# Kernel tuning notes

Hardware: AMD Instinct MI355X
Metric: run time of the kernel (lower is better)

Reference implementation:

```python
import jax, jax.numpy as jnp
import numpy as np

N_DRUG = 20000
N_DIS = 20000
D = 128
E = 640000
L = 200000


def _sage(x_src, x_dst, src, dst, Wl, Wr, b, n_dst):
    # SAGEConv: out_i = lin_l(mean_{j in N(i)} x_src_j) + lin_r(x_dst_i)
    msg = x_src[src]                                   # [E, D] gather
    agg = jax.ops.segment_sum(msg, dst, num_segments=n_dst)
    cnt = jax.ops.segment_sum(jnp.ones((src.shape[0],), x_src.dtype), dst,
                              num_segments=n_dst)
    mean = agg / jnp.maximum(cnt, 1.0)[:, None]
    return mean @ Wl + b + x_dst @ Wr


def setup_inputs() -> dict:
    key = jax.random.key(0)
    ks = jax.random.split(key, 24)
    s = 1.0 / np.sqrt(D)
    inp = {
        "x_drug": jax.random.normal(ks[0], (N_DRUG, D), jnp.float32),
        "x_disease": jax.random.normal(ks[1], (N_DIS, D), jnp.float32),
        "ei_d2s": jax.random.randint(ks[2], (2, E), 0, 20000),
        "ei_s2d": jax.random.randint(ks[3], (2, E), 0, 20000),
        "edge_label_index": jax.random.randint(ks[4], (2, L), 0, 20000),
    }
    names = ["W1l_d2s", "W1r_d2s", "W1l_s2d", "W1r_s2d",
             "W2l_d2s", "W2r_d2s", "W2l_s2d", "W2r_s2d"]
    for i, n in enumerate(names):
        inp[n] = jax.random.uniform(ks[5 + i], (D, D), jnp.float32, -s, s)
    for i, n in enumerate(["b1_d2s", "b1_s2d", "b2_d2s", "b2_s2d"]):
        inp[n] = jax.random.uniform(ks[13 + i], (D,), jnp.float32, -s, s)
    inp["dec_W1"] = jax.random.uniform(ks[17], (2 * D, D), jnp.float32, -s, s)
    inp["dec_b1"] = jax.random.uniform(ks[18], (D,), jnp.float32, -s, s)
    inp["dec_W2"] = jax.random.uniform(ks[19], (D, 1), jnp.float32, -s, s)
    inp["dec_b2"] = jax.random.uniform(ks[20], (1,), jnp.float32, -s, s)
    return inp


def reference(x_drug, x_disease,
              W1l_d2s, W1r_d2s, b1_d2s, W1l_s2d, W1r_s2d, b1_s2d,
              W2l_d2s, W2r_d2s, b2_d2s, W2l_s2d, W2r_s2d, b2_s2d,
              dec_W1, dec_b1, dec_W2, dec_b2,
              ei_d2s, ei_s2d, edge_label_index):
    # --- hetero GNN encoder, layer 1 (relu) ---
    h_dis = jax.nn.relu(_sage(x_drug, x_disease, ei_d2s[0], ei_d2s[1],
                              W1l_d2s, W1r_d2s, b1_d2s, N_DIS))
    h_drug = jax.nn.relu(_sage(x_disease, x_drug, ei_s2d[0], ei_s2d[1],
                               W1l_s2d, W1r_s2d, b1_s2d, N_DRUG))
    # --- layer 2 (no activation) ---
    z_dis = _sage(h_drug, h_dis, ei_d2s[0], ei_d2s[1],
                  W2l_d2s, W2r_d2s, b2_d2s, N_DIS)
    z_drug = _sage(h_dis, h_drug, ei_s2d[0], ei_s2d[1],
                   W2l_s2d, W2r_s2d, b2_s2d, N_DRUG)
    # --- edge decoder: gather, concat, 2-layer MLP ---
    row, col = edge_label_index[0], edge_label_index[1]
    z = jnp.concatenate([z_drug[row], z_dis[col]], axis=-1)   # [L, 2D]
    z = jax.nn.relu(z @ dec_W1 + dec_b1)
    z = z @ dec_W2 + dec_b2
    return z.reshape(-1)
```

## Files before the change

kernel.cpp:

```cpp
#include <hip/hip_runtime.h>
#include <hip/hip_fp16.h>

#define D 128
#define NDRUG 20000
#define NDIS 20000
#define EDGES 640000
#define LROWS 200000

typedef unsigned short u16;


__device__ inline void h8_load(uint4 u, float f[8]) {
    float2 a = __half22float2(*(const __half2*)&u.x);
    float2 b = __half22float2(*(const __half2*)&u.y);
    float2 c = __half22float2(*(const __half2*)&u.z);
    float2 d = __half22float2(*(const __half2*)&u.w);
    f[0] = a.x; f[1] = a.y; f[2] = b.x; f[3] = b.y;
    f[4] = c.x; f[5] = c.y; f[6] = d.x; f[7] = d.y;
}

__global__ __launch_bounds__(256) void rank2_kernel(
    const int* __restrict__ dA, int* __restrict__ cA, int* __restrict__ rA,
    const int* __restrict__ dB, int* __restrict__ cB, int* __restrict__ rB, int n)
{
    int i = blockIdx.x * blockDim.x + threadIdx.x;
    if (i < n) rA[i] = atomicAdd(&cA[dA[i]], 1);
    else if (i - n < n) rB[i - n] = atomicAdd(&cB[dB[i - n]], 1);
}

__global__ __launch_bounds__(1024) void scan2_kernel(int* __restrict__ c0, int* __restrict__ o0,
                                                     int* __restrict__ c1, int* __restrict__ o1,
                                                     int n) {
    int* cnt_io = (blockIdx.x == 0) ? c0 : c1;
    int* off    = (blockIdx.x == 0) ? o0 : o1;
    __shared__ int wsum[16];
    __shared__ int carry_s;
    const int tid = threadIdx.x;
    const int lane = tid & 63;
    const int wid = tid >> 6;
    if (tid == 0) { carry_s = 0; off[0] = 0; }
    __syncthreads();
    for (int start = 0; start < n; start += 1024) {
        int i = start + tid;
        int v = (i < n) ? cnt_io[i] : 0;
        int carry = carry_s;
        int s = v;
        #pragma unroll
        for (int o = 1; o < 64; o <<= 1) {
            int t = __shfl_up(s, o, 64);
            if (lane >= o) s += t;
        }
        if (lane == 63) wsum[wid] = s;
        __syncthreads();
        if (wid == 0) {
            int ws = (lane < 16) ? wsum[lane] : 0;
            #pragma unroll
            for (int o = 1; o < 16; o <<= 1) {
                int t = __shfl_up(ws, o, 64);
                if (lane >= o) ws += t;
            }
            if (lane < 16) wsum[lane] = ws;
        }
        __syncthreads();
        int woff = (wid > 0) ? wsum[wid - 1] : 0;
        int incl = s + woff + carry;
        if (i < n) {
            off[i + 1] = incl;
            cnt_io[i] = incl - v;
        }
        __syncthreads();
        if (tid == 1023) carry_s = incl;
        __syncthreads();
    }
}

#define SB 104

__global__ __launch_bounds__(256) void scatter_sliced_kernel(
    const int* __restrict__ srcA, const int* __restrict__ dstA,
    const int* __restrict__ rkA, const int* __restrict__ offA, u16* __restrict__ csrA,
    const int* __restrict__ srcB, const int* __restrict__ dstB,
    const int* __restrict__ rkB, const int* __restrict__ offB, u16* __restrict__ csrB,
    int n)
{
    int b = blockIdx.x;
    int dirB = (b >= 8 * SB);
    int bb = b - (dirB ? 8 * SB : 0);
    int s = bb & 7;
    int sub = bb >> 3;
    const int* src = dirB ? srcB : srcA;
    const int* dst = dirB ? dstB : dstA;
    const int* rk  = dirB ? rkB : rkA;
    const int* off = dirB ? offB : offA;
    u16* csr = dirB ? csrB : csrA;

    const int lo = s * 2500, hi = lo + 2500;
    const int chunk = (n + SB - 1) / SB;
    int i0 = sub * chunk;
    int i1 = i0 + chunk; i1 = i1 < n ? i1 : n;
    for (int i = i0 + threadIdx.x; i < i1; i += 256) {
        int d = dst[i];
        if (d >= lo && d < hi) {
            int pos = off[d] + rk[i];
            csr[pos] = (u16)src[i];
        }
    }
}


__global__ __launch_bounds__(256) void cvt16_kernel(const float* __restrict__ in,
                                                    __half* __restrict__ out, int n4) {
    int i = blockIdx.x * blockDim.x + threadIdx.x;
    if (i >= n4) return;
    float4 v = ((const float4*)in)[i];
    __half2 a = __floats2half2_rn(v.x, v.y);
    __half2 b = __floats2half2_rn(v.z, v.w);
    uint2 u;
    u.x = *(unsigned*)&a;
    u.y = *(unsigned*)&b;
    ((uint2*)out)[i] = u;
}

__global__ __launch_bounds__(256) void cvtw_kernel(
    const float* __restrict__ s0, const float* __restrict__ s1,
    const float* __restrict__ s2, const float* __restrict__ s3,
    const float* __restrict__ s4, const float* __restrict__ s5,
    const float* __restrict__ s6, const float* __restrict__ s7,
    const float* __restrict__ s8, const float* __restrict__ s9,
    __half* __restrict__ out)
{
    const int chunk = blockIdx.x >> 4;
    const float* src;
    switch (chunk) {
        case 0: src = s0; break; case 1: src = s1; break;
        case 2: src = s2; break; case 3: src = s3; break;
        case 4: src = s4; break; case 5: src = s5; break;
        case 6: src = s6; break; case 7: src = s7; break;
        case 8: src = s8; break; default: src = s9; break;
    }
    const int i4 = (blockIdx.x & 15) * 256 + threadIdx.x;
    float4 v = ((const float4*)src)[i4];
    __half2 a = __floats2half2_rn(v.x, v.y);
    __half2 b = __floats2half2_rn(v.z, v.w);
    uint2 u;
    u.x = *(unsigned*)&a;
    u.y = *(unsigned*)&b;
    ((uint2*)(out + (size_t)chunk * 16384))[i4] = u;
}


#define NPW 4

__device__ inline void sage_gather(
    const __half* __restrict__ xsrc, const __half* __restrict__ xdst,
    const int* __restrict__ off, const u16* __restrict__ csr,
    float lmean[4][NPW][D], float ldst[4][NPW][D],
    int node0, int ndst, int wid, int lane)
{
    const bool hiHalf = lane >= 32;
    const int lq = lane & 31;
    const int c0 = lq * 4;
    for (int r = 0; r < NPW; ++r) {
        int node = node0 + r;
        if (node >= ndst) break;
        int e0 = off[node], e1 = off[node + 1];
        int deg = e1 - e0;
        float a0 = 0.f, a1 = 0.f, a2 = 0.f, a3 = 0.f;
        for (int base = e0; base < e1; base += 64) {
            int nv = e1 - base; nv = nv < 64 ? nv : 64;
            int myidx = 0;
            if (lane < nv) myidx = csr[base + lane];
            int npair = nv >> 1;
            int t = 0;
            for (; t + 4 <= npair; t += 4) {
                int pa0 = __builtin_amdgcn_readlane(myidx, 2 * t + 0);
                int pb0 = __builtin_amdgcn_readlane(myidx, 2 * t + 1);
                int pa1 = __builtin_amdgcn_readlane(myidx, 2 * t + 2);
                int pb1 = __builtin_amdgcn_readlane(myidx, 2 * t + 3);
                int pa2 = __builtin_amdgcn_readlane(myidx, 2 * t + 4);
                int pb2 = __builtin_amdgcn_readlane(myidx, 2 * t + 5);
                int pa3 = __builtin_amdgcn_readlane(myidx, 2 * t + 6);
                int pb3 = __builtin_amdgcn_readlane(myidx, 2 * t + 7);
                int s0 = hiHalf ? pb0 : pa0;
                int s1 = hiHalf ? pb1 : pa1;
                int s2 = hiHalf ? pb2 : pa2;
                int s3 = hiHalf ? pb3 : pa3;
                uint2 u0 = *(const uint2*)(xsrc + (size_t)s0 * D + c0);
                uint2 u1 = *(const uint2*)(xsrc + (size_t)s1 * D + c0);
                uint2 u2 = *(const uint2*)(xsrc + (size_t)s2 * D + c0);
                uint2 u3 = *(const uint2*)(xsrc + (size_t)s3 * D + c0);
                float2 t0, t1;
                t0 = __half22float2(*(const __half2*)&u0.x);
                t1 = __half22float2(*(const __half2*)&u0.y);
                a0 += t0.x; a1 += t0.y; a2 += t1.x; a3 += t1.y;
                t0 = __half22float2(*(const __half2*)&u1.x);
                t1 = __half22float2(*(const __half2*)&u1.y);
                a0 += t0.x; a1 += t0.y; a2 += t1.x; a3 += t1.y;
                t0 = __half22float2(*(const __half2*)&u2.x);
                t1 = __half22float2(*(const __half2*)&u2.y);
                a0 += t0.x; a1 += t0.y; a2 += t1.x; a3 += t1.y;
                t0 = __half22float2(*(const __half2*)&u3.x);
                t1 = __half22float2(*(const __half2*)&u3.y);
                a0 += t0.x; a1 += t0.y; a2 += t1.x; a3 += t1.y;
            }
            for (; t < npair; ++t) {
                int pa = __builtin_amdgcn_readlane(myidx, 2 * t + 0);
                int pb = __builtin_amdgcn_readlane(myidx, 2 * t + 1);
                int s = hiHalf ? pb : pa;
                uint2 u = *(const uint2*)(xsrc + (size_t)s * D + c0);
                float2 t0 = __half22float2(*(const __half2*)&u.x);
                float2 t1 = __half22float2(*(const __half2*)&u.y);
                a0 += t0.x; a1 += t0.y; a2 += t1.x; a3 += t1.y;
            }
            if (nv & 1) {
                int s = __builtin_amdgcn_readlane(myidx, nv - 1);
                if (!hiHalf) {
                    uint2 u = *(const uint2*)(xsrc + (size_t)s * D + c0);
                    float2 t0 = __half22float2(*(const __half2*)&u.x);
                    float2 t1 = __half22float2(*(const __half2*)&u.y);
                    a0 += t0.x; a1 += t0.y; a2 += t1.x; a3 += t1.y;
                }
            }
        }
        a0 += __shfl_xor(a0, 32, 64);
        a1 += __shfl_xor(a1, 32, 64);
        a2 += __shfl_xor(a2, 32, 64);
        a3 += __shfl_xor(a3, 32, 64);
        float inv = 1.0f / (float)(deg < 1 ? 1 : deg);
        if (!hiHalf) {
            float4 m; m.x = a0 * inv; m.y = a1 * inv; m.z = a2 * inv; m.w = a3 * inv;
            *(float4*)&lmean[wid][r][c0] = m;
        } else {
            uint2 u = *(const uint2*)(xdst + (size_t)node * D + c0);
            float2 t0 = __half22float2(*(const __half2*)&u.x);
            float2 t1 = __half22float2(*(const __half2*)&u.y);
            float4 dv; dv.x = t0.x; dv.y = t0.y; dv.z = t1.x; dv.w = t1.y;
            *(float4*)&ldst[wid][r][c0] = dv;
        }
    }
}

__global__ __launch_bounds__(256, 4) void sage_l1_kernel(
    const __half* __restrict__ xsA, const __half* __restrict__ xdA,
    const int* __restrict__ offA, const u16* __restrict__ csrA,
    const __half* __restrict__ WlA, const __half* __restrict__ WrA,
    const float* __restrict__ bA, __half* __restrict__ outA, int nA, int blocksA,
    const __half* __restrict__ xsB, const __half* __restrict__ xdB,
    const int* __restrict__ offB, const u16* __restrict__ csrB,
    const __half* __restrict__ WlB, const __half* __restrict__ WrB,
    const float* __restrict__ bB, __half* __restrict__ outB, int nB)
{
    __shared__ __align__(16) float lmean[4][NPW][D];
    __shared__ __align__(16) float ldst[4][NPW][D];
    const bool bkB = (int)blockIdx.x >= blocksA;
    const int blk = bkB ? blockIdx.x - blocksA : blockIdx.x;
    const __half* xsrc = bkB ? xsB : xsA;
    const __half* xdst = bkB ? xdB : xdA;
    const int* off = bkB ? offB : offA;
    const u16* csr = bkB ? csrB : csrA;
    const __half* Wl = bkB ? WlB : WlA;
    const __half* Wr = bkB ? WrB : WrA;
    const float* b  = bkB ? bB : bA;
    __half* out16 = bkB ? outB : outA;
    const int ndst = bkB ? nB : nA;

    const int lane = threadIdx.x & 63;
    const int wid = threadIdx.x >> 6;
    const int j0 = lane * 2;
    const int node0 = (blk * 4 + wid) * NPW;

    sage_gather(xsrc, xdst, off, csr, lmean, ldst, node0, ndst, wid, lane);
    __syncthreads();

    float2 acc[NPW];
    float2 bv = *(const float2*)(b + j0);
    #pragma unroll
    for (int r = 0; r < NPW; ++r) acc[r] = bv;

    for (int k = 0; k < D; k += 2) {
        float2 wl0 = __half22float2(*(const __half2*)(Wl + (size_t)k * D + j0));
        float2 wr0 = __half22float2(*(const __half2*)(Wr + (size_t)k * D + j0));
        float2 wl1 = __half22float2(*(const __half2*)(Wl + (size_t)(k + 1) * D + j0));
        float2 wr1 = __half22float2(*(const __half2*)(Wr + (size_t)(k + 1) * D + j0));
        #pragma unroll
        for (int r = 0; r < NPW; ++r) {
            float2 m = *(const float2*)&lmean[wid][r][k];
            float2 dd = *(const float2*)&ldst[wid][r][k];
            acc[r].x = fmaf(m.x, wl0.x, acc[r].x);
            acc[r].y = fmaf(m.x, wl0.y, acc[r].y);
            acc[r].x = fmaf(dd.x, wr0.x, acc[r].x);
            acc[r].y = fmaf(dd.x, wr0.y, acc[r].y);
            acc[r].x = fmaf(m.y, wl1.x, acc[r].x);
            acc[r].y = fmaf(m.y, wl1.y, acc[r].y);
            acc[r].x = fmaf(dd.y, wr1.x, acc[r].x);
            acc[r].y = fmaf(dd.y, wr1.y, acc[r].y);
        }
    }

    for (int r = 0; r < NPW; ++r) {
        int node = node0 + r;
        if (node < ndst) {
            float ox = fmaxf(acc[r].x, 0.f), oy = fmaxf(acc[r].y, 0.f);
            __half2 hv = __floats2half2_rn(ox, oy);
            *(unsigned*)(out16 + (size_t)node * D + j0) = *(unsigned*)&hv;
        }
    }
}

__global__ __launch_bounds__(256, 4) void sage_l2_kernel(
    const __half* __restrict__ xsA, const __half* __restrict__ xdA,
    const int* __restrict__ offA, const u16* __restrict__ csrA,
    const __half* __restrict__ WlA, const __half* __restrict__ WrA,
    const float* __restrict__ bA, const __half* __restrict__ WdA,
    const float* __restrict__ pbA, __half* __restrict__ PoutA, int nA, int blocksA,
    const __half* __restrict__ xsB, const __half* __restrict__ xdB,
    const int* __restrict__ offB, const u16* __restrict__ csrB,
    const __half* __restrict__ WlB, const __half* __restrict__ WrB,
    const float* __restrict__ bB, const __half* __restrict__ WdB,
    const float* __restrict__ pbB, __half* __restrict__ PoutB, int nB)
{
    __shared__ __align__(16) float lmean[4][NPW][D];
    __shared__ __align__(16) float ldst[4][NPW][D];
    const bool bkB = (int)blockIdx.x >= blocksA;
    const int blk = bkB ? blockIdx.x - blocksA : blockIdx.x;
    const __half* xsrc = bkB ? xsB : xsA;
    const __half* xdst = bkB ? xdB : xdA;
    const int* off = bkB ? offB : offA;
    const u16* csr = bkB ? csrB : csrA;
    const __half* Wl = bkB ? WlB : WlA;
    const __half* Wr = bkB ? WrB : WrA;
    const float* b  = bkB ? bB : bA;
    const __half* Wd = bkB ? WdB : WdA;
    const float* pb = bkB ? pbB : pbA;
    __half* Pout = bkB ? PoutB : PoutA;
    const int ndst = bkB ? nB : nA;

    const int lane = threadIdx.x & 63;
    const int wid = threadIdx.x >> 6;
    const int j0 = lane * 2;
    const int node0 = (blk * 4 + wid) * NPW;

    sage_gather(xsrc, xdst, off, csr, lmean, ldst, node0, ndst, wid, lane);
    __syncthreads();

    float2 acc[NPW];
    float2 bv = *(const float2*)(b + j0);
    #pragma unroll
    for (int r = 0; r < NPW; ++r) acc[r] = bv;

    for (int k = 0; k < D; k += 2) {
        float2 wl0 = __half22float2(*(const __half2*)(Wl + (size_t)k * D + j0));
        float2 wr0 = __half22float2(*(const __half2*)(Wr + (size_t)k * D + j0));
        float2 wl1 = __half22float2(*(const __half2*)(Wl + (size_t)(k + 1) * D + j0));
        float2 wr1 = __half22float2(*(const __half2*)(Wr + (size_t)(k + 1) * D + j0));
        #pragma unroll
        for (int r = 0; r < NPW; ++r) {
            float2 m = *(const float2*)&lmean[wid][r][k];
            float2 dd = *(const float2*)&ldst[wid][r][k];
            acc[r].x = fmaf(m.x, wl0.x, acc[r].x);
            acc[r].y = fmaf(m.x, wl0.y, acc[r].y);
            acc[r].x = fmaf(dd.x, wr0.x, acc[r].x);
            acc[r].y = fmaf(dd.x, wr0.y, acc[r].y);
            acc[r].x = fmaf(m.y, wl1.x, acc[r].x);
            acc[r].y = fmaf(m.y, wl1.y, acc[r].y);
            acc[r].x = fmaf(dd.y, wr1.x, acc[r].x);
            acc[r].y = fmaf(dd.y, wr1.y, acc[r].y);
        }
    }

    __syncthreads();
    #pragma unroll
    for (int r = 0; r < NPW; ++r) {
        lmean[wid][r][j0] = acc[r].x;
        lmean[wid][r][j0 + 1] = acc[r].y;
    }
    __syncthreads();

    float2 pacc[NPW];
    float2 pbv;
    if (pb) pbv = *(const float2*)(pb + j0);
    else { pbv.x = 0.f; pbv.y = 0.f; }
    #pragma unroll
    for (int r = 0; r < NPW; ++r) pacc[r] = pbv;

    for (int k = 0; k < D; k += 2) {
        float2 wd0 = __half22float2(*(const __half2*)(Wd + (size_t)k * D + j0));
        float2 wd1 = __half22float2(*(const __half2*)(Wd + (size_t)(k + 1) * D + j0));
        #pragma unroll
        for (int r = 0; r < NPW; ++r) {
            float2 z = *(const float2*)&lmean[wid][r][k];
            pacc[r].x = fmaf(z.x, wd0.x, pacc[r].x);
            pacc[r].y = fmaf(z.x, wd0.y, pacc[r].y);
            pacc[r].x = fmaf(z.y, wd1.x, pacc[r].x);
            pacc[r].y = fmaf(z.y, wd1.y, pacc[r].y);
        }
    }

    for (int r = 0; r < NPW; ++r) {
        int node = node0 + r;
        if (node < ndst) {
            __half2 hv = __floats2half2_rn(pacc[r].x, pacc[r].y);
            *(unsigned*)(Pout + (size_t)node * D + j0) = *(unsigned*)&hv;
        }
    }
}


__global__ __launch_bounds__(256) void dec_gather_kernel(
    const __half* __restrict__ Pd, const __half* __restrict__ Ps,
    const int* __restrict__ row_idx, const int* __restrict__ col_idx,
    const float* __restrict__ W2, const float* __restrict__ b2,
    float* __restrict__ out, int nrows)
{
    const int lane = threadIdx.x & 63;
    const int wid = threadIdx.x >> 6;
    const int g = lane >> 4;
    const int lq = lane & 15;
    const int wave_id = blockIdx.x * 4 + wid;
    const int e0 = wave_id * 32;
    if (e0 >= nrows) return;

    const int c0 = lq * 8;
    float w2v[8];
    #pragma unroll
    for (int i = 0; i < 8; ++i) w2v[i] = W2[c0 + i];
    float b2v = b2[0];

    #pragma unroll 2
    for (int it = 0; it < 8; ++it) {
        int ei = it * 4 + g;
        int rr = e0 + ei;
        int ri = row_idx[rr];
        int ci = col_idx[rr];
        uint4 ua = *(const uint4*)(Pd + (size_t)ri * D + c0);
        uint4 ub = *(const uint4*)(Ps + (size_t)ci * D + c0);
        float fa[8], fb[8];
        h8_load(ua, fa);
        h8_load(ub, fb);
        float v = 0.f;
        #pragma unroll
        for (int i = 0; i < 8; ++i)
            v = fmaf(fmaxf(fa[i] + fb[i], 0.f), w2v[i], v);
        v += __shfl_xor(v, 1, 64);
        v += __shfl_xor(v, 2, 64);
        v += __shfl_xor(v, 4, 64);
        v += __shfl_xor(v, 8, 64);
        if (lq == 0) out[rr] = v + b2v;
    }
}


extern "C" void kernel_launch(void* const* d_in, const int* in_sizes, int n_in,
                              void* d_out, int out_size, void* d_ws, size_t ws_size,
                              hipStream_t stream) {
    const float* x_drug = (const float*)d_in[0];
    const float* x_dis  = (const float*)d_in[1];
    const int* ei_d2s = (const int*)d_in[2];
    const int* ei_s2d = (const int*)d_in[3];
    const int* ell    = (const int*)d_in[4];
    const float* W1l_d2s = (const float*)d_in[5];
    const float* W1r_d2s = (const float*)d_in[6];
    const float* W1l_s2d = (const float*)d_in[7];
    const float* W1r_s2d = (const float*)d_in[8];
    const float* W2l_d2s = (const float*)d_in[9];
    const float* W2r_d2s = (const float*)d_in[10];
    const float* W2l_s2d = (const float*)d_in[11];
    const float* W2r_s2d = (const float*)d_in[12];
    const float* b1_d2s = (const float*)d_in[13];
    const float* b1_s2d = (const float*)d_in[14];
    const float* b2_d2s = (const float*)d_in[15];
    const float* b2_s2d = (const float*)d_in[16];
    const float* dec_W1 = (const float*)d_in[17];
    const float* dec_b1 = (const float*)d_in[18];
    const float* dec_W2 = (const float*)d_in[19];
    const float* dec_b2 = (const float*)d_in[20];
    float* out = (float*)d_out;

    char* ws = (char*)d_ws;
    size_t o = 0;
    auto take = [&](size_t bytes) -> char* {
        char* p = ws + o;
        o += (bytes + 255) & ~(size_t)255;
        return p;
    };
    int* off_d2s = (int*)take((NDIS + 1) * sizeof(int));
    int* cnt_d2s = (int*)take(NDIS * sizeof(int));
    u16* csr_d2s = (u16*)take((size_t)EDGES * sizeof(u16));
    int* rk_d2s  = (int*)take((size_t)EDGES * sizeof(int));
    int* off_s2d = (int*)take((NDRUG + 1) * sizeof(int));
    int* cnt_s2d = (int*)take(NDRUG * sizeof(int));
    u16* csr_s2d = (u16*)take((size_t)EDGES * sizeof(u16));
    int* rk_s2d  = (int*)take((size_t)EDGES * sizeof(int));
    __half* x16_drug = (__half*)take((size_t)NDRUG * D * sizeof(__half));
    __half* x16_dis  = (__half*)take((size_t)NDIS * D * sizeof(__half));
    __half* h16_dis  = (__half*)take((size_t)NDIS * D * sizeof(__half));
    __half* h16_drug = (__half*)take((size_t)NDRUG * D * sizeof(__half));
    __half* P16_drug = (__half*)take((size_t)NDRUG * D * sizeof(__half));
    __half* P16_dis  = (__half*)take((size_t)NDIS * D * sizeof(__half));
    __half* w16 = (__half*)take((size_t)10 * 16384 * sizeof(__half));

    __half* w16_W1l_d2s = w16 + 0 * 16384;
    __half* w16_W1r_d2s = w16 + 1 * 16384;
    __half* w16_W1l_s2d = w16 + 2 * 16384;
    __half* w16_W1r_s2d = w16 + 3 * 16384;
    __half* w16_W2l_d2s = w16 + 4 * 16384;
    __half* w16_W2r_d2s = w16 + 5 * 16384;
    __half* w16_W2l_s2d = w16 + 6 * 16384;
    __half* w16_W2r_s2d = w16 + 7 * 16384;
    __half* w16_Wd_lo   = w16 + 8 * 16384;
    __half* w16_Wd_hi   = w16 + 9 * 16384;

    hipMemsetAsync(cnt_d2s, 0, NDIS * sizeof(int), stream);
    hipMemsetAsync(cnt_s2d, 0, NDRUG * sizeof(int), stream);

    cvtw_kernel<<<160, 256, 0, stream>>>(
        W1l_d2s, W1r_d2s, W1l_s2d, W1r_s2d,
        W2l_d2s, W2r_d2s, W2l_s2d, W2r_s2d,
        dec_W1, dec_W1 + 16384, w16);

    cvt16_kernel<<<(NDRUG * D / 4 + 255) / 256, 256, 0, stream>>>(x_drug, x16_drug, NDRUG * D / 4);
    cvt16_kernel<<<(NDIS * D / 4 + 255) / 256, 256, 0, stream>>>(x_dis, x16_dis, NDIS * D / 4);

    const int EB2 = (2 * EDGES + 255) / 256;
    rank2_kernel<<<EB2, 256, 0, stream>>>(ei_d2s + EDGES, cnt_d2s, rk_d2s,
                                          ei_s2d + EDGES, cnt_s2d, rk_s2d, EDGES);
    scan2_kernel<<<2, 1024, 0, stream>>>(cnt_d2s, off_d2s, cnt_s2d, off_s2d, NDIS);
    scatter_sliced_kernel<<<2 * 8 * SB, 256, 0, stream>>>(
        ei_d2s, ei_d2s + EDGES, rk_d2s, off_d2s, csr_d2s,
        ei_s2d, ei_s2d + EDGES, rk_s2d, off_s2d, csr_s2d, EDGES);

    const int BA = (NDIS + 4 * NPW - 1) / (4 * NPW);
    const int BB = (NDRUG + 4 * NPW - 1) / (4 * NPW);
    sage_l1_kernel<<<BA + BB, 256, 0, stream>>>(
        x16_drug, x16_dis, off_d2s, csr_d2s, w16_W1l_d2s, w16_W1r_d2s, b1_d2s, h16_dis, NDIS, BA,
        x16_dis, x16_drug, off_s2d, csr_s2d, w16_W1l_s2d, w16_W1r_s2d, b1_s2d, h16_drug, NDRUG);

    sage_l2_kernel<<<BA + BB, 256, 0, stream>>>(
        h16_drug, h16_dis, off_d2s, csr_d2s, w16_W2l_d2s, w16_W2r_d2s, b2_d2s,
        w16_Wd_hi, dec_b1, P16_dis, NDIS, BA,
        h16_dis, h16_drug, off_s2d, csr_s2d, w16_W2l_s2d, w16_W2r_s2d, b2_s2d,
        w16_Wd_lo, nullptr, P16_drug, NDRUG);

    dec_gather_kernel<<<(LROWS / 32 + 3) / 4, 256, 0, stream>>>(
        P16_drug, P16_dis, ell, ell + LROWS, dec_W2, dec_b2, out, LROWS);
}
```

Baseline: 305.8 us.

## Split neighbor mean aggregation into dimension-sliced kernel separate from matmul

Moves the per-node neighbor mean out of the fused SAGE kernels into a new mean16 kernel. In it, one thread owns a node and an 8-wide dimension slice and walks that node's CSR edges serially, writing a half-precision mean buffer. The matmul kernels then just load the precomputed mean and destination rows. The goal is better gather locality, since blocks share a dimension slice, and no wave-level readlane loops. The cost is two extra launches, an extra round trip of the mean through global memory, an extra fp16 rounding of the mean, and per-thread degree imbalance.

```diff
diff --git a/kernel.cpp b/kernel.cpp
--- a/kernel.cpp
+++ b/kernel.cpp
@@ -149,104 +149,56 @@
 }
 
 
+__global__ __launch_bounds__(256) void mean16_kernel(
+    const __half* __restrict__ xsA, const int* __restrict__ offA,
+    const u16* __restrict__ csrA, __half* __restrict__ mA, int nA, int blocksA,
+    const __half* __restrict__ xsB, const int* __restrict__ offB,
+    const u16* __restrict__ csrB, __half* __restrict__ mB, int nB)
+{
+    const bool bkB = (int)blockIdx.x >= blocksA;
+    const int bb = bkB ? blockIdx.x - blocksA : blockIdx.x;
+    const __half* xs = bkB ? xsB : xsA;
+    const int* off = bkB ? offB : offA;
+    const u16* csr = bkB ? csrB : csrA;
+    __half* mout = bkB ? mB : mA;
+    const int ndst = bkB ? nB : nA;
+
+    const int slice = bb & 15;
+    const int chunk = bb >> 4;
+    const int dimoff = slice * 8;
+    const int node = chunk * 256 + threadIdx.x;
+    if (node >= ndst) return;
+
+    int e0 = off[node], e1 = off[node + 1];
+    int deg = e1 - e0;
+    float a[8] = {0.f, 0.f, 0.f, 0.f, 0.f, 0.f, 0.f, 0.f};
+    for (int e = e0; e < e1; ++e) {
+        int s = csr[e];
+        uint4 u = *(const uint4*)(xs + (size_t)s * D + dimoff);
+        float f[8];
+        h8_load(u, f);
+        #pragma unroll
+        for (int i = 0; i < 8; ++i) a[i] += f[i];
+    }
+    float inv = 1.0f / (float)(deg < 1 ? 1 : deg);
+    __half2 h0 = __floats2half2_rn(a[0] * inv, a[1] * inv);
+    __half2 h1 = __floats2half2_rn(a[2] * inv, a[3] * inv);
+    __half2 h2 = __floats2half2_rn(a[4] * inv, a[5] * inv);
+    __half2 h3 = __floats2half2_rn(a[6] * inv, a[7] * inv);
+    uint4 o;
+    o.x = *(unsigned*)&h0; o.y = *(unsigned*)&h1;
+    o.z = *(unsigned*)&h2; o.w = *(unsigned*)&h3;
+    *(uint4*)(mout + (size_t)node * D + dimoff) = o;
+}
+
+
 #define NPW 4
 
-__device__ inline void sage_gather(
-    const __half* __restrict__ xsrc, const __half* __restrict__ xdst,
-    const int* __restrict__ off, const u16* __restrict__ csr,
-    float lmean[4][NPW][D], float ldst[4][NPW][D],
-    int node0, int ndst, int wid, int lane)
-{
-    const bool hiHalf = lane >= 32;
-    const int lq = lane & 31;
-    const int c0 = lq * 4;
-    for (int r = 0; r < NPW; ++r) {
-        int node = node0 + r;
-        if (node >= ndst) break;
-        int e0 = off[node], e1 = off[node + 1];
-        int deg = e1 - e0;
-        float a0 = 0.f, a1 = 0.f, a2 = 0.f, a3 = 0.f;
-        for (int base = e0; base < e1; base += 64) {
-            int nv = e1 - base; nv = nv < 64 ? nv : 64;
-            int myidx = 0;
-            if (lane < nv) myidx = csr[base + lane];
-            int npair = nv >> 1;
-            int t = 0;
-            for (; t + 4 <= npair; t += 4) {
-                int pa0 = __builtin_amdgcn_readlane(myidx, 2 * t + 0);
-                int pb0 = __builtin_amdgcn_readlane(myidx, 2 * t + 1);
-                int pa1 = __builtin_amdgcn_readlane(myidx, 2 * t + 2);
-                int pb1 = __builtin_amdgcn_readlane(myidx, 2 * t + 3);
-                int pa2 = __builtin_amdgcn_readlane(myidx, 2 * t + 4);
-                int pb2 = __builtin_amdgcn_readlane(myidx, 2 * t + 5);
-                int pa3 = __builtin_amdgcn_readlane(myidx, 2 * t + 6);
-                int pb3 = __builtin_amdgcn_readlane(myidx, 2 * t + 7);
-                int s0 = hiHalf ? pb0 : pa0;
-                int s1 = hiHalf ? pb1 : pa1;
-                int s2 = hiHalf ? pb2 : pa2;
-                int s3 = hiHalf ? pb3 : pa3;
-                uint2 u0 = *(const uint2*)(xsrc + (size_t)s0 * D + c0);
-                uint2 u1 = *(const uint2*)(xsrc + (size_t)s1 * D + c0);
-                uint2 u2 = *(const uint2*)(xsrc + (size_t)s2 * D + c0);
-                uint2 u3 = *(const uint2*)(xsrc + (size_t)s3 * D + c0);
-                float2 t0, t1;
-                t0 = __half22float2(*(const __half2*)&u0.x);
-                t1 = __half22float2(*(const __half2*)&u0.y);
-                a0 += t0.x; a1 += t0.y; a2 += t1.x; a3 += t1.y;
-                t0 = __half22float2(*(const __half2*)&u1.x);
-                t1 = __half22float2(*(const __half2*)&u1.y);
-                a0 += t0.x; a1 += t0.y; a2 += t1.x; a3 += t1.y;
-                t0 = __half22float2(*(const __half2*)&u2.x);
-                t1 = __half22float2(*(const __half2*)&u2.y);
-                a0 += t0.x; a1 += t0.y; a2 += t1.x; a3 += t1.y;
-                t0 = __half22float2(*(const __half2*)&u3.x);
-                t1 = __half22float2(*(const __half2*)&u3.y);
-                a0 += t0.x; a1 += t0.y; a2 += t1.x; a3 += t1.y;
-            }
-            for (; t < npair; ++t) {
-                int pa = __builtin_amdgcn_readlane(myidx, 2 * t + 0);
-                int pb = __builtin_amdgcn_readlane(myidx, 2 * t + 1);
-                int s = hiHalf ? pb : pa;
-                uint2 u = *(const uint2*)(xsrc + (size_t)s * D + c0);
-                float2 t0 = __half22float2(*(const __half2*)&u.x);
-                float2 t1 = __half22float2(*(const __half2*)&u.y);
-                a0 += t0.x; a1 += t0.y; a2 += t1.x; a3 += t1.y;
-            }
-            if (nv & 1) {
-                int s = __builtin_amdgcn_readlane(myidx, nv - 1);
-                if (!hiHalf) {
-                    uint2 u = *(const uint2*)(xsrc + (size_t)s * D + c0);
-                    float2 t0 = __half22float2(*(const __half2*)&u.x);
-                    float2 t1 = __half22float2(*(const __half2*)&u.y);
-                    a0 += t0.x; a1 += t0.y; a2 += t1.x; a3 += t1.y;
-                }
-            }
-        }
-        a0 += __shfl_xor(a0, 32, 64);
-        a1 += __shfl_xor(a1, 32, 64);
-        a2 += __shfl_xor(a2, 32, 64);
-        a3 += __shfl_xor(a3, 32, 64);
-        float inv = 1.0f / (float)(deg < 1 ? 1 : deg);
-        if (!hiHalf) {
-            float4 m; m.x = a0 * inv; m.y = a1 * inv; m.z = a2 * inv; m.w = a3 * inv;
-            *(float4*)&lmean[wid][r][c0] = m;
-        } else {
-            uint2 u = *(const uint2*)(xdst + (size_t)node * D + c0);
-            float2 t0 = __half22float2(*(const __half2*)&u.x);
-            float2 t1 = __half22float2(*(const __half2*)&u.y);
-            float4 dv; dv.x = t0.x; dv.y = t0.y; dv.z = t1.x; dv.w = t1.y;
-            *(float4*)&ldst[wid][r][c0] = dv;
-        }
-    }
-}
-
-__global__ __launch_bounds__(256, 4) void sage_l1_kernel(
-    const __half* __restrict__ xsA, const __half* __restrict__ xdA,
-    const int* __restrict__ offA, const u16* __restrict__ csrA,
+__global__ __launch_bounds__(256, 4) void mm_l1_kernel(
+    const __half* __restrict__ mnA, const __half* __restrict__ xdA,
     const __half* __restrict__ WlA, const __half* __restrict__ WrA,
     const float* __restrict__ bA, __half* __restrict__ outA, int nA, int blocksA,
-    const __half* __restrict__ xsB, const __half* __restrict__ xdB,
-    const int* __restrict__ offB, const u16* __restrict__ csrB,
+    const __half* __restrict__ mnB, const __half* __restrict__ xdB,
     const __half* __restrict__ WlB, const __half* __restrict__ WrB,
     const float* __restrict__ bB, __half* __restrict__ outB, int nB)
 {
@@ -254,10 +206,8 @@
     __shared__ __align__(16) float ldst[4][NPW][D];
     const bool bkB = (int)blockIdx.x >= blocksA;
     const int blk = bkB ? blockIdx.x - blocksA : blockIdx.x;
-    const __half* xsrc = bkB ? xsB : xsA;
+    const __half* mn = bkB ? mnB : mnA;
     const __half* xdst = bkB ? xdB : xdA;
-    const int* off = bkB ? offB : offA;
-    const u16* csr = bkB ? csrB : csrA;
     const __half* Wl = bkB ? WlB : WlA;
     const __half* Wr = bkB ? WrB : WrA;
     const float* b  = bkB ? bB : bA;
@@ -269,7 +219,14 @@
     const int j0 = lane * 2;
     const int node0 = (blk * 4 + wid) * NPW;
 
-    sage_gather(xsrc, xdst, off, csr, lmean, ldst, node0, ndst, wid, lane);
+    for (int r = 0; r < NPW; ++r) {
+        int node = node0 + r;
+        if (node >= ndst) break;
+        float2 mv = __half22float2(*(const __half2*)(mn + (size_t)node * D + j0));
+        lmean[wid][r][j0] = mv.x; lmean[wid][r][j0 + 1] = mv.y;
+        float2 xf = __half22float2(*(const __half2*)(xdst + (size_t)node * D + j0));
+        ldst[wid][r][j0] = xf.x; ldst[wid][r][j0 + 1] = xf.y;
+    }
     __syncthreads();
 
     float2 acc[NPW];
@@ -307,14 +264,12 @@
     }
 }
 
-__global__ __launch_bounds__(256, 4) void sage_l2_kernel(
-    const __half* __restrict__ xsA, const __half* __restrict__ xdA,
-    const int* __restrict__ offA, const u16* __restrict__ csrA,
+__global__ __launch_bounds__(256, 4) void mm_l2_kernel(
+    const __half* __restrict__ mnA, const __half* __restrict__ xdA,
     const __half* __restrict__ WlA, const __half* __restrict__ WrA,
     const float* __restrict__ bA, const __half* __restrict__ WdA,
     const float* __restrict__ pbA, __half* __restrict__ PoutA, int nA, int blocksA,
-    const __half* __restrict__ xsB, const __half* __restrict__ xdB,
-    const int* __restrict__ offB, const u16* __restrict__ csrB,
+    const __half* __restrict__ mnB, const __half* __restrict__ xdB,
     const __half* __restrict__ WlB, const __half* __restrict__ WrB,
     const float* __restrict__ bB, const __half* __restrict__ WdB,
     const float* __restrict__ pbB, __half* __restrict__ PoutB, int nB)
@@ -323,10 +278,8 @@
     __shared__ __align__(16) float ldst[4][NPW][D];
     const bool bkB = (int)blockIdx.x >= blocksA;
     const int blk = bkB ? blockIdx.x - blocksA : blockIdx.x;
-    const __half* xsrc = bkB ? xsB : xsA;
+    const __half* mn = bkB ? mnB : mnA;
     const __half* xdst = bkB ? xdB : xdA;
-    const int* off = bkB ? offB : offA;
-    const u16* csr = bkB ? csrB : csrA;
     const __half* Wl = bkB ? WlB : WlA;
     const __half* Wr = bkB ? WrB : WrA;
     const float* b  = bkB ? bB : bA;
@@ -340,7 +293,14 @@
     const int j0 = lane * 2;
     const int node0 = (blk * 4 + wid) * NPW;
 
-    sage_gather(xsrc, xdst, off, csr, lmean, ldst, node0, ndst, wid, lane);
+    for (int r = 0; r < NPW; ++r) {
+        int node = node0 + r;
+        if (node >= ndst) break;
+        float2 mv = __half22float2(*(const __half2*)(mn + (size_t)node * D + j0));
+        lmean[wid][r][j0] = mv.x; lmean[wid][r][j0 + 1] = mv.y;
+        float2 xf = __half22float2(*(const __half2*)(xdst + (size_t)node * D + j0));
+        ldst[wid][r][j0] = xf.x; ldst[wid][r][j0 + 1] = xf.y;
+    }
     __syncthreads();
 
     float2 acc[NPW];
@@ -497,6 +457,8 @@
     __half* h16_drug = (__half*)take((size_t)NDRUG * D * sizeof(__half));
     __half* P16_drug = (__half*)take((size_t)NDRUG * D * sizeof(__half));
     __half* P16_dis  = (__half*)take((size_t)NDIS * D * sizeof(__half));
+    __half* mean_dis  = (__half*)take((size_t)NDIS * D * sizeof(__half));
+    __half* mean_drug = (__half*)take((size_t)NDRUG * D * sizeof(__half));
     __half* w16 = (__half*)take((size_t)10 * 16384 * sizeof(__half));
 
     __half* w16_W1l_d2s = w16 + 0 * 16384;
@@ -529,16 +491,26 @@
         ei_d2s, ei_d2s + EDGES, rk_d2s, off_d2s, csr_d2s,
         ei_s2d, ei_s2d + EDGES, rk_s2d, off_s2d, csr_s2d, EDGES);
 
+    const int MCH_A = (NDIS + 255) / 256;
+    const int MCH_B = (NDRUG + 255) / 256;
+    const int MBA = MCH_A * 16, MBB = MCH_B * 16;
     const int BA = (NDIS + 4 * NPW - 1) / (4 * NPW);
     const int BB = (NDRUG + 4 * NPW - 1) / (4 * NPW);
-    sage_l1_kernel<<<BA + BB, 256, 0, stream>>>(
-        x16_drug, x16_dis, off_d2s, csr_d2s, w16_W1l_d2s, w16_W1r_d2s, b1_d2s, h16_dis, NDIS, BA,
-        x16_dis, x16_drug, off_s2d, csr_s2d, w16_W1l_s2d, w16_W1r_s2d, b1_s2d, h16_drug, NDRUG);
-
-    sage_l2_kernel<<<BA + BB, 256, 0, stream>>>(
-        h16_drug, h16_dis, off_d2s, csr_d2s, w16_W2l_d2s, w16_W2r_d2s, b2_d2s,
+
+    mean16_kernel<<<MBA + MBB, 256, 0, stream>>>(
+        x16_drug, off_d2s, csr_d2s, mean_dis, NDIS, MBA,
+        x16_dis, off_s2d, csr_s2d, mean_drug, NDRUG);
+    mm_l1_kernel<<<BA + BB, 256, 0, stream>>>(
+        mean_dis, x16_dis, w16_W1l_d2s, w16_W1r_d2s, b1_d2s, h16_dis, NDIS, BA,
+        mean_drug, x16_drug, w16_W1l_s2d, w16_W1r_s2d, b1_s2d, h16_drug, NDRUG);
+
+    mean16_kernel<<<MBA + MBB, 256, 0, stream>>>(
+        h16_drug, off_d2s, csr_d2s, mean_dis, NDIS, MBA,
+        h16_dis, off_s2d, csr_s2d, mean_drug, NDRUG);
+    mm_l2_kernel<<<BA + BB, 256, 0, stream>>>(
+        mean_dis, h16_dis, w16_W2l_d2s, w16_W2r_d2s, b2_d2s,
         w16_Wd_hi, dec_b1, P16_dis, NDIS, BA,
-        h16_dis, h16_drug, off_s2d, csr_s2d, w16_W2l_s2d, w16_W2r_s2d, b2_s2d,
+        mean_drug, h16_drug, w16_W2l_s2d, w16_W2r_s2d, b2_s2d,
         w16_Wd_lo, nullptr, P16_drug, NDRUG);
 
     dec_gather_kernel<<<(LROWS / 32 + 3) / 4, 256, 0, stream>>>(
```

Result: slower. 864.8 us (+182.8%).
